# Optimization experiments

Measured on AMD Instinct MI355X. Metric: run time of the kernel, lower is better.

Reference implementation:

```python
import jax, jax.numpy as jnp
import numpy as np

NEG_INF = -1e9

def setup_inputs() -> dict:
    key = jax.random.key(0)
    ks = jax.random.split(key, 7)
    B, NQ, NK, DQ, DK, DV, DH = 16, 128, 2048, 256, 256, 128, 64
    queries = jax.random.normal(ks[0], (B, NQ, DQ), dtype=jnp.float32)
    keys = jax.random.normal(ks[1], (B, NK, DK), dtype=jnp.float32)
    values = jax.random.normal(ks[2], (B, NK, DV), dtype=jnp.float32)
    valid_lens = jax.random.randint(ks[3], (B,), 1, NK + 1, dtype=jnp.int32)
    Wq = jax.random.normal(ks[4], (DQ, DH), dtype=jnp.float32) / np.sqrt(DQ)
    Wk = jax.random.normal(ks[5], (DK, DH), dtype=jnp.float32) / np.sqrt(DK)
    wv = jax.random.normal(ks[6], (DH,), dtype=jnp.float32) / np.sqrt(DH)
    return {"queries": queries, "keys": keys, "values": values,
            "valid_lens": valid_lens, "Wq": Wq, "Wk": Wk, "wv": wv}


def reference(queries, keys, values, valid_lens, Wq, Wk, wv):
    # Additive (Bahdanau) attention.
    q = jnp.einsum('bqd,dh->bqh', queries, Wq)   # [B, nq, dH]
    k = jnp.einsum('bkd,dh->bkh', keys, Wk)      # [B, nk, dH]
    # broadcast add -> tanh -> reduce with wv: scores [B, nq, nk]
    feat = jnp.tanh(q[:, :, None, :] + k[:, None, :, :])  # [B, nq, nk, dH]
    scores = jnp.einsum('bqkh,h->bqk', feat, wv)
    # masked softmax over nk using per-batch valid lengths
    nk = keys.shape[1]
    mask = jnp.arange(nk)[None, None, :] < valid_lens[:, None, None]  # [B,1,nk]
    scores = jnp.where(mask, scores, NEG_INF)
    attn = jax.nn.softmax(scores, axis=-1)
    # dropout is identity at eval time
    return jnp.einsum('bqk,bkv->bqv', attn, values)  # [B, nq, dv]
```

## Files before the change

### kernel.cpp

```cpp
#include <hip/hip_runtime.h>
#include <stddef.h>


__device__ __forceinline__ float fast_rcp(float x)  { return __builtin_amdgcn_rcpf(x); }
__device__ __forceinline__ float fast_exp2(float x) { return __builtin_amdgcn_exp2f(x); }

#define C2F 2.88539008177792681f
#define L2E 1.44269504088896340f

#if __has_builtin(__builtin_amdgcn_global_load_lds)
#define HAS_GLL 1
__device__ __forceinline__ void gload_lds16(const void* gsrc, void* ldst) {
  __builtin_amdgcn_global_load_lds(
      (const __attribute__((address_space(1))) unsigned int*)gsrc,
      (__attribute__((address_space(3))) unsigned int*)ldst, 16, 0, 0);
}
#else
#define HAS_GLL 0
#endif

#define M_CNTS 0
#define M_NS   1
#define M_PSC  32

__global__ void init_kernel(const int* __restrict__ vlens, int* __restrict__ meta)
{
  if (threadIdx.x == 0) {
    int as = 0;
    meta[M_PSC] = 0;
    for (int b = 0; b < 16; ++b) {
      as += (vlens[b] + 127) >> 7;
      meta[M_PSC + 1 + b] = as;
    }
    meta[M_NS]   = as * 8;
    meta[M_CNTS] = 0;
  }
}

template<int MODE>
__device__ __forceinline__
void proj_body(const float* __restrict__ inb, const float* __restrict__ W,
               float* __restrict__ out, const float* __restrict__ wv,
               int b, int r0, int rowsPerB, int t)
{
  __shared__ float4 Wlds[256 * 16];
  __shared__ float  klds[64 * 36];

  const float4* W4 = (const float4*)W;
#if HAS_GLL
  {
    float4* wdst = Wlds + (t & ~63);
    #pragma unroll
    for (int i = 0; i < 16; ++i)
      gload_lds16(W4 + t + 256 * i, wdst + 256 * i);
  }
#else
  #pragma unroll
  for (int i = 0; i < 16; ++i) Wlds[t + 256 * i] = W4[t + 256 * i];
#endif

  const int j = t >> 4;
  const int g = t & 15;

  float acc[4][4];
  #pragma unroll
  for (int m = 0; m < 4; ++m)
    acc[m][0] = acc[m][1] = acc[m][2] = acc[m][3] = 0.f;

  for (int dc = 0; dc < 8; ++dc) {
    {
      const int row = t >> 2, cs = (t & 3) * 8;
      const float* s = inb + row * 256 + dc * 32 + cs;
      float4 a0 = *(const float4*)s;
      float4 a1 = *(const float4*)(s + 4);
      float* dst = &klds[row * 36 + cs];
      *(float4*)dst       = a0;
      *(float4*)(dst + 4) = a1;
    }
    __syncthreads();
    #pragma unroll
    for (int d = 0; d < 32; ++d) {
      float4 w4 = Wlds[(dc * 32 + d) * 16 + j];
      #pragma unroll
      for (int m = 0; m < 4; ++m) {
        float kv = klds[(g + 16 * m) * 36 + d];
        acc[m][0] = fmaf(kv, w4.x, acc[m][0]);
        acc[m][1] = fmaf(kv, w4.y, acc[m][1]);
        acc[m][2] = fmaf(kv, w4.z, acc[m][2]);
        acc[m][3] = fmaf(kv, w4.w, acc[m][3]);
      }
    }
    __syncthreads();
  }

  if constexpr (MODE == 1) {
    #pragma unroll
    for (int m = 0; m < 4; ++m) {
      int k = r0 + g + 16 * m;
      size_t base = ((size_t)(b * 16 + (k >> 7)) * 64) * 128 + (k & 127);
      #pragma unroll
      for (int i = 0; i < 4; ++i)
        out[base + (size_t)(4 * j + i) * 128] = fast_exp2(C2F * acc[m][i]);
    }
  } else if constexpr (MODE == 2) {
    #pragma unroll
    for (int m = 0; m < 4; ++m) {
      int k = r0 + g + 16 * m;
      size_t base = (size_t)(b * 16 + (k >> 7)) * 8192 + (size_t)(k & 127) * 2;
      float e0 = fast_exp2(C2F * acc[m][0]);
      float e1 = fast_exp2(C2F * acc[m][1]);
      float e2 = fast_exp2(C2F * acc[m][2]);
      float e3 = fast_exp2(C2F * acc[m][3]);
      *(float2*)&out[base + (size_t)(2 * j) * 256]     = make_float2(e0, e1);
      *(float2*)&out[base + (size_t)(2 * j + 1) * 256] = make_float2(e2, e3);
    }
  } else if constexpr (MODE == 3) {
    float4 wq = ((const float4*)wv)[j];
    #pragma unroll
    for (int m = 0; m < 4; ++m) {
      int row = r0 + g + 16 * m;
      float e0 = fast_exp2(C2F * acc[m][0]);
      float e1 = fast_exp2(C2F * acc[m][1]);
      float e2 = fast_exp2(C2F * acc[m][2]);
      float e3 = fast_exp2(C2F * acc[m][3]);
      float4* dst = (float4*)out + ((size_t)(b * 128 + row)) * 32;
      dst[2 * j]     = make_float4(e0, e1, -2.f * wq.x, -2.f * wq.y);
      dst[2 * j + 1] = make_float4(e2, e3, -2.f * wq.z, -2.f * wq.w);
    }
  } else {
    #pragma unroll
    for (int m = 0; m < 4; ++m) {
      int row = r0 + g + 16 * m;
      float4 o;
      o.x = fast_exp2(C2F * acc[m][0]);
      o.y = fast_exp2(C2F * acc[m][1]);
      o.z = fast_exp2(C2F * acc[m][2]);
      o.w = fast_exp2(C2F * acc[m][3]);
      *(float4*)&out[((size_t)b * rowsPerB + row) * 64 + 4 * j] = o;
    }
  }
}

__global__ __launch_bounds__(256)
void proj_qk_kernel(const float* __restrict__ queries, const float* __restrict__ keys,
                    const float* __restrict__ Wq, const float* __restrict__ Wk,
                    float* __restrict__ EqW, float* __restrict__ EkP,
                    const float* __restrict__ wv, const int* __restrict__ vlens)
{
  const int blk = blockIdx.x;
  if (blk >= 512) {
    const int idx = blk - 512;
    const int b = idx & 15, rt = idx >> 4, r0 = rt * 64;
    proj_body<3>(queries + ((size_t)b * 128 + r0) * 256, Wq, EqW, wv, b, r0, 128,
                 threadIdx.x);
  } else {
    const int b = blk & 15, rt = blk >> 4, r0 = rt * 64;
    if (r0 >= vlens[b]) return;
    proj_body<2>(keys + ((size_t)b * 2048 + r0) * 256, Wk, EkP, wv, b, r0, 2048,
                 threadIdx.x);
  }
}

template<int MODE, bool CHECK>
__global__ __launch_bounds__(256)
void proj_kernel(const float* __restrict__ in, const float* __restrict__ W,
                 float* __restrict__ out, const int* __restrict__ vlens,
                 int rowsPerB)
{
  const int t  = threadIdx.x;
  const int b  = blockIdx.x & 15;
  const int rt = blockIdx.x >> 4;
  const int r0 = rt * 64;
  if constexpr (CHECK) {
    if (r0 >= vlens[b]) return;
  }
  proj_body<MODE>(in + ((size_t)b * rowsPerB + r0) * 256, W, out,
                  (const float*)nullptr, b, r0, rowsPerB, t);
}

__global__ __launch_bounds__(512, 6)
void scorepv_kernel(const float* __restrict__ EqW, const float* __restrict__ EkP,
                    const float* __restrict__ values, const int* __restrict__ vlens,
                    const float* __restrict__ wv,
                    float* __restrict__ partial, float* __restrict__ tsum,
                    int* __restrict__ meta)
{
  __shared__ float ek_lds[8192];
  __shared__ float eqw_lds[2048];
  __shared__ float p_lds[128 * 20];
  __shared__ int sh_u, sh_pre[17];

  const int t = threadIdx.x;
  if (t < 17) sh_pre[t] = meta[M_PSC + t];
  const int nunits = meta[M_NS];

  float W1 = 0.f, w0 = 0.f;
  #pragma unroll
  for (int u = 0; u < 16; ++u) {
    float4 v = ((const float4*)wv)[u];
    w0 += v.x + v.y + v.z + v.w;
    W1 += fabsf(v.x) + fabsf(v.y) + fabsf(v.z) + fabsf(v.w);
  }

  const int wave_u = __builtin_amdgcn_readfirstlane(t >> 6);
  const int lane   = t & 63;
  const int kp     = lane * 2;
  const int q0l    = wave_u * 2;

  for (;;) {
    __syncthreads();
    if (t == 0) sh_u = atomicAdd(&meta[M_CNTS], 1);
    __syncthreads();
    const int u = sh_u;
    if (u >= nunits) break;

    const int w  = u >> 3;
    const int qq = u & 7;
    int b = 0;
    while (w >= sh_pre[1 + b]) ++b;
    const int kt = w - sh_pre[b];
    const int vl = vlens[b];

    {
      const float4* src  = (const float4*)(EkP + (size_t)(b * 16 + kt) * 8192);
      const float4* qsrc = (const float4*)EqW + ((size_t)(b * 128 + qq * 16)) * 32;
#if HAS_GLL
      float4* dstw = (float4*)ek_lds + (t & ~63);
      #pragma unroll
      for (int i = 0; i < 4; ++i)
        gload_lds16(src + t + 512 * i, dstw + 512 * i);
      gload_lds16(qsrc + t, (float4*)eqw_lds + (t & ~63));
#else
      float4* dst = (float4*)ek_lds;
      #pragma unroll
      for (int i = 0; i < 4; ++i) dst[t + 512 * i] = src[t + 512 * i];
      ((float4*)eqw_lds)[t] = qsrc[t];
#endif
    }
    __syncthreads();

    float s[2][2] = {{w0, w0}, {w0, w0}};
    const float4* ek4 = (const float4*)ek_lds;
    const float4* eqw = (const float4*)eqw_lds;
    #pragma unroll 8
    for (int hp = 0; hp < 32; ++hp) {
      float4 e = ek4[hp * 64 + lane];
      #pragma unroll
      for (int q = 0; q < 2; ++q) {
        float4 ew = eqw[(q0l + q) * 32 + hp];
        { float x0 = fmaf(ew.x, e.x, 1.f), x1 = fmaf(ew.y, e.y, 1.f);
          float y = fast_rcp(x0 * x1);
          float a = ew.w * x0; a = fmaf(ew.z, x1, a);
          s[q][0] = fmaf(a, y, s[q][0]); }
        { float x0 = fmaf(ew.x, e.z, 1.f), x1 = fmaf(ew.y, e.w, 1.f);
          float y = fast_rcp(x0 * x1);
          float a = ew.w * x0; a = fmaf(ew.z, x1, a);
          s[q][1] = fmaf(a, y, s[q][1]); }
      }
    }

    const int kbase = kt * 128 + kp;
    float p[2][2];
    #pragma unroll
    for (int q = 0; q < 2; ++q) {
      p[q][0] = (kbase     < vl) ? fast_exp2((s[q][0] - W1) * L2E) : 0.f;
      p[q][1] = (kbase + 1 < vl) ? fast_exp2((s[q][1] - W1) * L2E) : 0.f;
    }

    *(float2*)&p_lds[kp * 20 + q0l]       = make_float2(p[0][0], p[1][0]);
    *(float2*)&p_lds[(kp + 1) * 20 + q0l] = make_float2(p[0][1], p[1][1]);

    const int q0g = qq * 16 + q0l;
    #pragma unroll
    for (int q = 0; q < 2; ++q) {
      float e = p[q][0] + p[q][1];
      #pragma unroll
      for (int m = 1; m < 64; m <<= 1) e += __shfl_xor(e, m, 64);
      if (lane == 0) tsum[(size_t)(b * 16 + kt) * 128 + q0g + q] = e;
    }
    __syncthreads();

    const int kg = t >> 7, v = t & 127;
    const int kloc = min(128, vl - kt * 128);
    const int k0 = kg * 32, k1 = min(k0 + 32, kloc);
    const int len = (k1 > k0) ? (k1 - k0) : 0;
    const int nfull = len & ~7;
    const float* vb = values + ((size_t)(b * 2048 + kt * 128)) * 128 + v;
    float acc[16];
    #pragma unroll
    for (int i = 0; i < 16; ++i) acc[i] = 0.f;

    for (int kb = k0; kb < k0 + nfull; kb += 8) {
      float vv[8];
      #pragma unroll
      for (int j = 0; j < 8; ++j) vv[j] = vb[(size_t)(kb + j) * 128];
      #pragma unroll
      for (int j = 0; j < 8; ++j) {
        const float* pr = &p_lds[(kb + j) * 20];
        float4 p0 = *(const float4*)&pr[0];
        float4 p1 = *(const float4*)&pr[4];
        float4 p2 = *(const float4*)&pr[8];
        float4 p3 = *(const float4*)&pr[12];
        float vx = vv[j];
        acc[ 0]=fmaf(p0.x,vx,acc[ 0]); acc[ 1]=fmaf(p0.y,vx,acc[ 1]);
        acc[ 2]=fmaf(p0.z,vx,acc[ 2]); acc[ 3]=fmaf(p0.w,vx,acc[ 3]);
        acc[ 4]=fmaf(p1.x,vx,acc[ 4]); acc[ 5]=fmaf(p1.y,vx,acc[ 5]);
        acc[ 6]=fmaf(p1.z,vx,acc[ 6]); acc[ 7]=fmaf(p1.w,vx,acc[ 7]);
        acc[ 8]=fmaf(p2.x,vx,acc[ 8]); acc[ 9]=fmaf(p2.y,vx,acc[ 9]);
        acc[10]=fmaf(p2.z,vx,acc[10]); acc[11]=fmaf(p2.w,vx,acc[11]);
        acc[12]=fmaf(p3.x,vx,acc[12]); acc[13]=fmaf(p3.y,vx,acc[13]);
        acc[14]=fmaf(p3.z,vx,acc[14]); acc[15]=fmaf(p3.w,vx,acc[15]);
      }
    }
    for (int k = k0 + nfull; k < k1; ++k) {
      float vx = vb[(size_t)k * 128];
      const float* pr = &p_lds[k * 20];
      #pragma unroll
      for (int q = 0; q < 16; ++q) acc[q] = fmaf(pr[q], vx, acc[q]);
    }

    __syncthreads();
    float* red = ek_lds;
    if (kg > 0) {
      #pragma unroll
      for (int q = 0; q < 16; ++q) red[(kg - 1) * 2048 + q * 128 + v] = acc[q];
    }
    __syncthreads();
    if (kg == 0) {
      #pragma unroll
      for (int q = 0; q < 16; ++q) {
        float tot = acc[q] + red[q * 128 + v] + red[2048 + q * 128 + v]
                  + red[4096 + q * 128 + v];
        partial[(((size_t)(b * 128 + qq * 16 + q)) * 16 + kt) * 128 + v] = tot;
      }
    }
  }
}

__global__ __launch_bounds__(256)
void reduce_kernel(const float* __restrict__ partial, const float* __restrict__ tsum,
                   const int* __restrict__ vlens, float* __restrict__ out)
{
  const int blk = blockIdx.x;
  const int b   = blk >> 6;
  const int q   = (blk & 63) * 2 + (threadIdx.x >> 7);
  const int v   = threadIdx.x & 127;
  const int ntk = (vlens[b] + 127) >> 7;

  float tot = 0.f;
  for (int i = 0; i < ntk; ++i)
    tot += tsum[(size_t)(b * 16 + i) * 128 + q];

  float acc = 0.f;
  const float* pp = partial + ((size_t)(b * 128 + q)) * 16 * 128 + v;
  for (int i = 0; i < ntk; ++i)
    acc += pp[(size_t)i * 128];

  out[((size_t)(b * 128 + q)) * 128 + v] = acc / tot;
}

__global__ __launch_bounds__(256)
void attn_kernel(const float* __restrict__ Eq, const float* __restrict__ EkT,
                 const float* __restrict__ values, const int* __restrict__ vlens,
                 const float* __restrict__ wv, float* __restrict__ out)
{
  const int t    = threadIdx.x;
  const int b    = blockIdx.x & 15;
  const int qt   = blockIdx.x >> 4;
  const int wave = t >> 6;
  const int lane = t & 63;

  __shared__ float4 sc4[512 * 4];
  __shared__ float  pvp[128 * 5];
  __shared__ float  linvs[4];

  const int vl = vlens[b];

  float eqv[64], wv2[64];
  float w0 = 0.f;
  {
    const float4* eq4 = (const float4*)(Eq + (size_t)(b * 128 + qt * 4 + wave) * 64);
    const float4* wv4 = (const float4*)wv;
    #pragma unroll
    for (int u = 0; u < 16; ++u) {
      float4 e = eq4[u], v = wv4[u];
      eqv[4*u+0] = e.x; eqv[4*u+1] = e.y; eqv[4*u+2] = e.z; eqv[4*u+3] = e.w;
      wv2[4*u+0] = -2.f * v.x; wv2[4*u+1] = -2.f * v.y;
      wv2[4*u+2] = -2.f * v.z; wv2[4*u+3] = -2.f * v.w;
      w0 += v.x + v.y + v.z + v.w;
    }
  }

  const int ktiles = (vl + 127) >> 7;
  const int kp = 2 * lane;
  for (int kt = 0; kt < ktiles; ++kt) {
    const float* tb = EkT + ((size_t)(b * 16 + kt) * 64) * 128 + kp;
    float s0 = w0, s1 = w0;
    #pragma unroll
    for (int h = 0; h < 64; ++h) {
      float2 ek = *(const float2*)(tb + (size_t)h * 128);
      float r0 = fast_rcp(fmaf(eqv[h], ek.x, 1.0f));
      float r1 = fast_rcp(fmaf(eqv[h], ek.y, 1.0f));
      s0 = fmaf(wv2[h], r0, s0);
      s1 = fmaf(wv2[h], r1, s1);
    }
    int k = kt * 128 + kp;
    if (k     >= vl) s0 = -1e9f;
    if (k + 1 >= vl) s1 = -1e9f;
    float* scf = (float*)sc4;
    *(float2*)(scf + (((k >> 2) * 4 + wave) * 4 + (k & 3))) = make_float2(s0, s1);
  }

  const int nq4 = (vl + 3) >> 2;
  float mx = -3e38f;
  for (int Q = lane; Q < nq4; Q += 64) {
    float4 f = sc4[Q * 4 + wave];
    mx = fmaxf(mx, fmaxf(fmaxf(f.x, f.y), fmaxf(f.z, f.w)));
  }
  #pragma unroll
  for (int msk = 1; msk < 64; msk <<= 1) mx = fmaxf(mx, __shfl_xor(mx, msk, 64));
  float lsum = 0.f;
  for (int Q = lane; Q < nq4; Q += 64) {
    float4 f = sc4[Q * 4 + wave];
    f.x = fast_exp2((f.x - mx) * L2E);
    f.y = fast_exp2((f.y - mx) * L2E);
    f.z = fast_exp2((f.z - mx) * L2E);
    f.w = fast_exp2((f.w - mx) * L2E);
    sc4[Q * 4 + wave] = f;
    lsum += f.x + f.y + f.z + f.w;
  }
  #pragma unroll
  for (int msk = 1; msk < 64; msk <<= 1) lsum += __shfl_xor(lsum, msk, 64);
  if (lane == 0) linvs[wave] = fast_rcp(lsum);
  __syncthreads();

  const int grp = t >> 7, v = t & 127;
  float acc[4] = {0.f, 0.f, 0.f, 0.f};
  const float* vb = values + (size_t)b * 2048 * 128 + v;
  for (int Q = grp; Q < nq4; Q += 2) {
    float4 p0 = sc4[Q * 4 + 0], p1 = sc4[Q * 4 + 1];
    float4 p2 = sc4[Q * 4 + 2], p3 = sc4[Q * 4 + 3];
    const float* vk = vb + (size_t)(Q * 4) * 128;
    float x;
    x = vk[0];
    acc[0]=fmaf(p0.x,x,acc[0]); acc[1]=fmaf(p1.x,x,acc[1]);
    acc[2]=fmaf(p2.x,x,acc[2]); acc[3]=fmaf(p3.x,x,acc[3]);
    x = vk[128];
    acc[0]=fmaf(p0.y,x,acc[0]); acc[1]=fmaf(p1.y,x,acc[1]);
    acc[2]=fmaf(p2.y,x,acc[2]); acc[3]=fmaf(p3.y,x,acc[3]);
    x = vk[256];
    acc[0]=fmaf(p0.z,x,acc[0]); acc[1]=fmaf(p1.z,x,acc[1]);
    acc[2]=fmaf(p2.z,x,acc[2]); acc[3]=fmaf(p3.z,x,acc[3]);
    x = vk[384];
    acc[0]=fmaf(p0.w,x,acc[0]); acc[1]=fmaf(p1.w,x,acc[1]);
    acc[2]=fmaf(p2.w,x,acc[2]); acc[3]=fmaf(p3.w,x,acc[3]);
  }
  if (grp == 1) {
    #pragma unroll
    for (int qq = 0; qq < 4; ++qq) pvp[v * 5 + qq] = acc[qq];
  }
  __syncthreads();
  if (grp == 0) {
    #pragma unroll
    for (int qq = 0; qq < 4; ++qq) {
      float tot = acc[qq] + pvp[v * 5 + qq];
      out[((size_t)(b * 128) + qt * 4 + qq) * 128 + v] = tot * linvs[qq];
    }
  }
}

extern "C" void kernel_launch(void* const* d_in, const int* in_sizes, int n_in,
                              void* d_out, int out_size, void* d_ws, size_t ws_size,
                              hipStream_t stream) {
  const float* queries = (const float*)d_in[0];
  const float* keys    = (const float*)d_in[1];
  const float* values  = (const float*)d_in[2];
  const int*   vlens   = (const int*)d_in[3];
  const float* Wq      = (const float*)d_in[4];
  const float* Wk      = (const float*)d_in[5];
  const float* wv      = (const float*)d_in[6];
  float* outp = (float*)d_out;

  float* base    = (float*)d_ws;
  float* EqW     = base;
  float* EkP     = base + 262144;
  float* tsumb   = base + 2359296;
  float* partial = base + 2392064;
  int*   meta    = (int*)(base + 6586368);
  const size_t need = (size_t)6586368 * 4 + 256;

  if (ws_size >= need) {
    hipLaunchKernelGGL(init_kernel, dim3(1), dim3(64), 0, stream, vlens, meta);
    hipLaunchKernelGGL(proj_qk_kernel, dim3(544), dim3(256), 0, stream,
                       queries, keys, Wq, Wk, EqW, EkP, wv, vlens);
    hipLaunchKernelGGL(scorepv_kernel, dim3(768), dim3(512), 0, stream,
                       EqW, EkP, values, vlens, wv, partial, tsumb, meta);
    hipLaunchKernelGGL(reduce_kernel, dim3(1024), dim3(256), 0, stream,
                       partial, tsumb, vlens, outp);
  } else {
    hipLaunchKernelGGL((proj_kernel<0, false>), dim3(32), dim3(256), 0, stream,
                       queries, Wq, EqW, (const int*)nullptr, 128);
    hipLaunchKernelGGL((proj_kernel<1, true>), dim3(512), dim3(256), 0, stream,
                       keys, Wk, EkP, vlens, 2048);
    hipLaunchKernelGGL(attn_kernel, dim3(512), dim3(256), 0, stream,
                       EqW, EkP, values, vlens, wv, outp);
  }
}
```

Baseline: 83.20 us.

## Double queries per work unit in scorepv and fold init into projection kernel

Each scorepv work unit now covers 32 queries instead of 16, so every loaded key tile and value row is reused across twice as many queries. The number of units halves, and the query-weight staging buffer is merged into the enlarged probability LDS buffer. The separate init kernel is removed and its metadata setup is done by an extra block of the projection kernel, which saves one launch. In exchange each thread keeps 32 accumulators, so register pressure rises against the launch bound of 6, and there are fewer units to spread across the CUs.

```diff
diff --git a/kernel.cpp b/kernel.cpp
--- a/kernel.cpp
+++ b/kernel.cpp
@@ -22,20 +22,6 @@
 #define M_CNTS 0
 #define M_NS   1
 #define M_PSC  32
-
-__global__ void init_kernel(const int* __restrict__ vlens, int* __restrict__ meta)
-{
-  if (threadIdx.x == 0) {
-    int as = 0;
-    meta[M_PSC] = 0;
-    for (int b = 0; b < 16; ++b) {
-      as += (vlens[b] + 127) >> 7;
-      meta[M_PSC + 1 + b] = as;
-    }
-    meta[M_NS]   = as * 8;
-    meta[M_CNTS] = 0;
-  }
-}
 
 template<int MODE>
 __device__ __forceinline__
@@ -145,9 +131,23 @@
 void proj_qk_kernel(const float* __restrict__ queries, const float* __restrict__ keys,
                     const float* __restrict__ Wq, const float* __restrict__ Wk,
                     float* __restrict__ EqW, float* __restrict__ EkP,
-                    const float* __restrict__ wv, const int* __restrict__ vlens)
+                    const float* __restrict__ wv, const int* __restrict__ vlens,
+                    int* __restrict__ meta)
 {
   const int blk = blockIdx.x;
+  if (blk == 544) {
+    if (threadIdx.x == 0) {
+      int as = 0;
+      meta[M_PSC] = 0;
+      for (int b = 0; b < 16; ++b) {
+        as += (vlens[b] + 127) >> 7;
+        meta[M_PSC + 1 + b] = as;
+      }
+      meta[M_NS]   = as * 4;
+      meta[M_CNTS] = 0;
+    }
+    return;
+  }
   if (blk >= 512) {
     const int idx = blk - 512;
     const int b = idx & 15, rt = idx >> 4, r0 = rt * 64;
@@ -186,8 +186,7 @@
                     int* __restrict__ meta)
 {
   __shared__ float ek_lds[8192];
-  __shared__ float eqw_lds[2048];
-  __shared__ float p_lds[128 * 20];
+  __shared__ float p_lds[128 * 36];
   __shared__ int sh_u, sh_pre[17];
 
   const int t = threadIdx.x;
@@ -205,7 +204,7 @@
   const int wave_u = __builtin_amdgcn_readfirstlane(t >> 6);
   const int lane   = t & 63;
   const int kp     = lane * 2;
-  const int q0l    = wave_u * 2;
+  const int q0l    = wave_u * 4;
 
   for (;;) {
     __syncthreads();
@@ -214,8 +213,8 @@
     const int u = sh_u;
     if (u >= nunits) break;
 
-    const int w  = u >> 3;
-    const int qq = u & 7;
+    const int w  = u >> 2;
+    const int qq = u & 3;
     int b = 0;
     while (w >= sh_pre[1 + b]) ++b;
     const int kt = w - sh_pre[b];
@@ -223,30 +222,36 @@
 
     {
       const float4* src  = (const float4*)(EkP + (size_t)(b * 16 + kt) * 8192);
-      const float4* qsrc = (const float4*)EqW + ((size_t)(b * 128 + qq * 16)) * 32;
+      const float4* qsrc = (const float4*)EqW + ((size_t)(b * 128 + qq * 32)) * 32;
 #if HAS_GLL
       float4* dstw = (float4*)ek_lds + (t & ~63);
       #pragma unroll
       for (int i = 0; i < 4; ++i)
         gload_lds16(src + t + 512 * i, dstw + 512 * i);
-      gload_lds16(qsrc + t, (float4*)eqw_lds + (t & ~63));
+      float4* pdstw = (float4*)p_lds + (t & ~63);
+      gload_lds16(qsrc + t,       pdstw);
+      gload_lds16(qsrc + t + 512, pdstw + 512);
 #else
       float4* dst = (float4*)ek_lds;
       #pragma unroll
       for (int i = 0; i < 4; ++i) dst[t + 512 * i] = src[t + 512 * i];
-      ((float4*)eqw_lds)[t] = qsrc[t];
+      ((float4*)p_lds)[t]       = qsrc[t];
+      ((float4*)p_lds)[t + 512] = qsrc[t + 512];
 #endif
     }
     __syncthreads();
 
-    float s[2][2] = {{w0, w0}, {w0, w0}};
+    float s[4][2];
+    #pragma unroll
+    for (int q = 0; q < 4; ++q) { s[q][0] = w0; s[q][1] = w0; }
+
     const float4* ek4 = (const float4*)ek_lds;
-    const float4* eqw = (const float4*)eqw_lds;
-    #pragma unroll 8
+    const float4* eqw = (const float4*)p_lds;
+    #pragma unroll 4
     for (int hp = 0; hp < 32; ++hp) {
       float4 e = ek4[hp * 64 + lane];
       #pragma unroll
-      for (int q = 0; q < 2; ++q) {
+      for (int q = 0; q < 4; ++q) {
         float4 ew = eqw[(q0l + q) * 32 + hp];
         { float x0 = fmaf(ew.x, e.x, 1.f), x1 = fmaf(ew.y, e.y, 1.f);
           float y = fast_rcp(x0 * x1);
@@ -260,24 +265,25 @@
     }
 
     const int kbase = kt * 128 + kp;
-    float p[2][2];
-    #pragma unroll
-    for (int q = 0; q < 2; ++q) {
+    float p[4][2];
+    #pragma unroll
+    for (int q = 0; q < 4; ++q) {
       p[q][0] = (kbase     < vl) ? fast_exp2((s[q][0] - W1) * L2E) : 0.f;
       p[q][1] = (kbase + 1 < vl) ? fast_exp2((s[q][1] - W1) * L2E) : 0.f;
     }
 
-    *(float2*)&p_lds[kp * 20 + q0l]       = make_float2(p[0][0], p[1][0]);
-    *(float2*)&p_lds[(kp + 1) * 20 + q0l] = make_float2(p[0][1], p[1][1]);
-
-    const int q0g = qq * 16 + q0l;
-    #pragma unroll
-    for (int q = 0; q < 2; ++q) {
+    const int q0g = qq * 32 + q0l;
+    #pragma unroll
+    for (int q = 0; q < 4; ++q) {
       float e = p[q][0] + p[q][1];
       #pragma unroll
       for (int m = 1; m < 64; m <<= 1) e += __shfl_xor(e, m, 64);
       if (lane == 0) tsum[(size_t)(b * 16 + kt) * 128 + q0g + q] = e;
     }
+
+    __syncthreads();
+    *(float4*)&p_lds[kp * 36 + q0l]       = make_float4(p[0][0], p[1][0], p[2][0], p[3][0]);
+    *(float4*)&p_lds[(kp + 1) * 36 + q0l] = make_float4(p[0][1], p[1][1], p[2][1], p[3][1]);
     __syncthreads();
 
     const int kg = t >> 7, v = t & 127;
@@ -286,9 +292,9 @@
     const int len = (k1 > k0) ? (k1 - k0) : 0;
     const int nfull = len & ~7;
     const float* vb = values + ((size_t)(b * 2048 + kt * 128)) * 128 + v;
-    float acc[16];
-    #pragma unroll
-    for (int i = 0; i < 16; ++i) acc[i] = 0.f;
+    float acc[32];
+    #pragma unroll
+    for (int i = 0; i < 32; ++i) acc[i] = 0.f;
 
     for (int kb = k0; kb < k0 + nfull; kb += 8) {
       float vv[8];
@@ -296,42 +302,43 @@
       for (int j = 0; j < 8; ++j) vv[j] = vb[(size_t)(kb + j) * 128];
       #pragma unroll
       for (int j = 0; j < 8; ++j) {
-        const float* pr = &p_lds[(kb + j) * 20];
-        float4 p0 = *(const float4*)&pr[0];
-        float4 p1 = *(const float4*)&pr[4];
-        float4 p2 = *(const float4*)&pr[8];
-        float4 p3 = *(const float4*)&pr[12];
+        const float4* pr = (const float4*)&p_lds[(kb + j) * 36];
         float vx = vv[j];
-        acc[ 0]=fmaf(p0.x,vx,acc[ 0]); acc[ 1]=fmaf(p0.y,vx,acc[ 1]);
-        acc[ 2]=fmaf(p0.z,vx,acc[ 2]); acc[ 3]=fmaf(p0.w,vx,acc[ 3]);
-        acc[ 4]=fmaf(p1.x,vx,acc[ 4]); acc[ 5]=fmaf(p1.y,vx,acc[ 5]);
-        acc[ 6]=fmaf(p1.z,vx,acc[ 6]); acc[ 7]=fmaf(p1.w,vx,acc[ 7]);
-        acc[ 8]=fmaf(p2.x,vx,acc[ 8]); acc[ 9]=fmaf(p2.y,vx,acc[ 9]);
-        acc[10]=fmaf(p2.z,vx,acc[10]); acc[11]=fmaf(p2.w,vx,acc[11]);
-        acc[12]=fmaf(p3.x,vx,acc[12]); acc[13]=fmaf(p3.y,vx,acc[13]);
-        acc[14]=fmaf(p3.z,vx,acc[14]); acc[15]=fmaf(p3.w,vx,acc[15]);
+        #pragma unroll
+        for (int qg = 0; qg < 8; ++qg) {
+          float4 pq = pr[qg];
+          acc[4*qg+0] = fmaf(pq.x, vx, acc[4*qg+0]);
+          acc[4*qg+1] = fmaf(pq.y, vx, acc[4*qg+1]);
+          acc[4*qg+2] = fmaf(pq.z, vx, acc[4*qg+2]);
+          acc[4*qg+3] = fmaf(pq.w, vx, acc[4*qg+3]);
+        }
       }
     }
     for (int k = k0 + nfull; k < k1; ++k) {
       float vx = vb[(size_t)k * 128];
-      const float* pr = &p_lds[k * 20];
-      #pragma unroll
-      for (int q = 0; q < 16; ++q) acc[q] = fmaf(pr[q], vx, acc[q]);
-    }
-
-    __syncthreads();
-    float* red = ek_lds;
-    if (kg > 0) {
-      #pragma unroll
-      for (int q = 0; q < 16; ++q) red[(kg - 1) * 2048 + q * 128 + v] = acc[q];
+      const float* pr = &p_lds[k * 36];
+      #pragma unroll
+      for (int q = 0; q < 32; ++q) acc[q] = fmaf(pr[q], vx, acc[q]);
+    }
+
+    __syncthreads();
+    if (kg == 1) {
+      #pragma unroll
+      for (int q = 0; q < 32; ++q) ek_lds[q * 128 + v] = acc[q];
+    } else if (kg == 2) {
+      #pragma unroll
+      for (int q = 0; q < 32; ++q) ek_lds[4096 + q * 128 + v] = acc[q];
+    } else if (kg == 3) {
+      #pragma unroll
+      for (int q = 0; q < 32; ++q) p_lds[q * 128 + v] = acc[q];
     }
     __syncthreads();
     if (kg == 0) {
       #pragma unroll
-      for (int q = 0; q < 16; ++q) {
-        float tot = acc[q] + red[q * 128 + v] + red[2048 + q * 128 + v]
-                  + red[4096 + q * 128 + v];
-        partial[(((size_t)(b * 128 + qq * 16 + q)) * 16 + kt) * 128 + v] = tot;
+      for (int q = 0; q < 32; ++q) {
+        float tot = acc[q] + ek_lds[q * 128 + v] + ek_lds[4096 + q * 128 + v]
+                  + p_lds[q * 128 + v];
+        partial[(((size_t)(b * 128 + qq * 32 + q)) * 16 + kt) * 128 + v] = tot;
       }
     }
   }
@@ -490,9 +497,8 @@
   const size_t need = (size_t)6586368 * 4 + 256;
 
   if (ws_size >= need) {
-    hipLaunchKernelGGL(init_kernel, dim3(1), dim3(64), 0, stream, vlens, meta);
-    hipLaunchKernelGGL(proj_qk_kernel, dim3(544), dim3(256), 0, stream,
-                       queries, keys, Wq, Wk, EqW, EkP, wv, vlens);
+    hipLaunchKernelGGL(proj_qk_kernel, dim3(545), dim3(256), 0, stream,
+                       queries, keys, Wq, Wk, EqW, EkP, wv, vlens, meta);
     hipLaunchKernelGGL(scorepv_kernel, dim3(768), dim3(512), 0, stream,
                        EqW, EkP, values, vlens, wv, partial, tsumb, meta);
     hipLaunchKernelGGL(reduce_kernel, dim3(1024), dim3(256), 0, stream,
```

Measured after the change: 85.48 us. 2.7% more time.
